# Optimization experiments

Hardware: AMD Instinct MI355X
Metric: run time of the kernel (lower is better)

## Reference

```python
import jax, jax.numpy as jnp
import numpy as np

B, D_IN, UNITS = 8192, 4096, 4096

def setup_inputs() -> dict:
    key = jax.random.key(0)
    k1, k2 = jax.random.split(key)
    x = jax.random.normal(k1, (B, D_IN), dtype=jnp.float32)
    w = jax.random.normal(k2, (D_IN, UNITS), dtype=jnp.float32)
    b = jnp.zeros((UNITS,), dtype=jnp.float32)
    return {"x": x, "w": w, "b": b}

def reference(x, w, b):
    # Bipolar dense: sign-binarize the weights, full-precision matmul, bias, relu.
    weights = jnp.sign(w)  # values in {-1, 0, +1}; matches tf.math.sign
    out = jnp.matmul(x, weights) + b  # [B, UNITS]
    return jax.nn.relu(out)
```

## Files before the change

kernel.cpp:

```cpp
#include <hip/hip_runtime.h>
#include <hip/hip_bf16.h>
#include <stdint.h>

#define M_DIM 8192
#define N_DIM 4096
#define K_DIM 4096

typedef __attribute__((ext_vector_type(4))) int   int4v;
typedef __attribute__((ext_vector_type(4))) float floatx4;

__global__ __launch_bounds__(256) void quant_x_kernel(const float* __restrict__ x,
                                                      signed char* __restrict__ xq,
                                                      float* __restrict__ xs) {
    const int row = blockIdx.x;
    const int tid = threadIdx.x;
    const int wave = tid >> 6, lane = tid & 63;
    const float4* xr = (const float4*)(x + (size_t)row * K_DIM);

    float4 v[4];
    float m = 0.f;
    #pragma unroll
    for (int j = 0; j < 4; ++j) {
        v[j] = xr[j * 256 + tid];
        m = fmaxf(m, fmaxf(fmaxf(fabsf(v[j].x), fabsf(v[j].y)),
                           fmaxf(fabsf(v[j].z), fabsf(v[j].w))));
    }
    #pragma unroll
    for (int off = 32; off >= 1; off >>= 1) m = fmaxf(m, __shfl_down(m, off));
    __shared__ float wm[4];
    if (lane == 0) wm[wave] = m;
    __syncthreads();
    const float M = fmaxf(fmaxf(wm[0], wm[1]), fmaxf(wm[2], wm[3]));
    const float inv = M > 0.f ? 127.f / M : 0.f;
    if (tid == 0) xs[row] = M > 0.f ? M / 127.f : 0.f;

    char4* xo = (char4*)(xq + (size_t)row * K_DIM);
    #pragma unroll
    for (int j = 0; j < 4; ++j) {
        char4 q;
        q.x = (signed char)__float2int_rn(v[j].x * inv);
        q.y = (signed char)__float2int_rn(v[j].y * inv);
        q.z = (signed char)__float2int_rn(v[j].z * inv);
        q.w = (signed char)__float2int_rn(v[j].w * inv);
        xo[j * 256 + tid] = q;
    }
}

__global__ __launch_bounds__(256) void cvt_w_kernel(const float* __restrict__ w,
                                                    signed char* __restrict__ wT) {
    __shared__ signed char tile[64][68];
    const int t  = threadIdx.x;
    const int k0 = blockIdx.y * 64;
    const int n0 = blockIdx.x * 64;
    #pragma unroll
    for (int p = 0; p < 4; ++p) {
        int kk = p * 16 + (t >> 4);
        int nn = (t & 15) * 4;
        float4 v = *reinterpret_cast<const float4*>(&w[(size_t)(k0 + kk) * N_DIM + n0 + nn]);
        tile[kk][nn + 0] = v.x > 0.f ? 1 : (v.x < 0.f ? -1 : 0);
        tile[kk][nn + 1] = v.y > 0.f ? 1 : (v.y < 0.f ? -1 : 0);
        tile[kk][nn + 2] = v.z > 0.f ? 1 : (v.z < 0.f ? -1 : 0);
        tile[kk][nn + 3] = v.w > 0.f ? 1 : (v.w < 0.f ? -1 : 0);
    }
    __syncthreads();
    const int r = t >> 2;
    const int c = (t & 3) * 16;
    int4v o;
    signed char* op = (signed char*)&o;
    #pragma unroll
    for (int j = 0; j < 16; ++j) op[j] = tile[c + j][r];
    *reinterpret_cast<int4v*>(&wT[(size_t)(n0 + r) * K_DIM + k0 + c]) = o;
}

#define BM 256
#define BN 256
#define BK 64
#define NT (K_DIM / BK)

#define GLD(gsrc, ldst) __builtin_amdgcn_global_load_lds( \
    (const __attribute__((address_space(1))) unsigned int*)(gsrc), \
    (__attribute__((address_space(3))) unsigned int*)(ldst), 16, 0, 0)

__global__ __launch_bounds__(512, 2) void gemm_i8_kernel(
    const signed char* __restrict__ A,
    const signed char* __restrict__ BT,
    const float* __restrict__ xsc,
    const float* __restrict__ bias,
    float* __restrict__ C)
{
    __shared__ signed char As[3][2][128 * 64];
    __shared__ signed char Bs[3][2][128 * 64];

    const int tid  = threadIdx.x;
    const int wave = tid >> 6;
    const int lane = tid & 63;
    const int wm   = wave >> 2;
    const int wn   = wave & 3;
    const int bh   = wn >> 1;
    const int brow0 = (wn & 1) * 64;

    const int bid  = blockIdx.x;
    const int sbid = (bid & 7) * 64 + (bid >> 3);
    const int tn   = sbid & 15;
    const int tm   = sbid >> 4;
    const int bm   = tm * BM;
    const int bn   = tn * BN;

    const int srow = tid >> 2;
    const int scol = ((tid & 3) ^ ((tid >> 3) & 3)) * 16;

    const int laneRow = (lane & 15) * 64;
    const int colX = ((lane >> 4) * 16) ^ (((lane >> 1) & 3) << 4);

    int4v acc[8][4] = {};

#define STAGE_HALF(G, R0, KOFS, LDST) do { \
    GLD((G) + (size_t)((R0) + srow) * K_DIM + (KOFS) + scol, (LDST) + wave * 1024); \
  } while (0)

    STAGE_HALF(A,  bm,        0, As[0][0]);
    STAGE_HALF(A,  bm + 128,  0, As[0][1]);
    STAGE_HALF(BT, bn,        0, Bs[0][0]);
    STAGE_HALF(BT, bn + 128,  0, Bs[0][1]);
    STAGE_HALF(A,  bm,       BK, As[1][0]);
    STAGE_HALF(A,  bm + 128, BK, As[1][1]);
    STAGE_HALF(BT, bn,       BK, Bs[1][0]);
    STAGE_HALF(BT, bn + 128, BK, Bs[1][1]);
    asm volatile("s_waitcnt vmcnt(4)" ::: "memory");
    __builtin_amdgcn_s_barrier();

    int4v a[4];
    int4v a2[4];
    int4v b[4];

    int rd = 0;
    int st = 2;

    for (int t = 0; t < NT; ++t) {
        const char* Ar = (const char*)As[rd][wm];
        const char* Br = (const char*)Bs[rd][bh];
        const int kS = (t + 2 < NT ? t + 2 : NT - 1) * BK;

        a[0]  = *(const int4v*)(Ar + (0*16)*64 + laneRow + colX);
        b[0]  = *(const int4v*)(Br + (brow0 +  0)*64 + laneRow + colX);
        b[1]  = *(const int4v*)(Br + (brow0 + 16)*64 + laneRow + colX);
        b[2]  = *(const int4v*)(Br + (brow0 + 32)*64 + laneRow + colX);
        b[3]  = *(const int4v*)(Br + (brow0 + 48)*64 + laneRow + colX);
        a[1]  = *(const int4v*)(Ar + (1*16)*64 + laneRow + colX);
        a[2]  = *(const int4v*)(Ar + (2*16)*64 + laneRow + colX);
        a[3]  = *(const int4v*)(Ar + (3*16)*64 + laneRow + colX);
        a2[0] = *(const int4v*)(Ar + ((64 + 0*16))*64 + laneRow + colX);
        a2[1] = *(const int4v*)(Ar + ((64 + 1*16))*64 + laneRow + colX);
        a2[2] = *(const int4v*)(Ar + ((64 + 2*16))*64 + laneRow + colX);
        a2[3] = *(const int4v*)(Ar + ((64 + 3*16))*64 + laneRow + colX);

        STAGE_HALF(A,  bm,       kS, As[st][0]);
        STAGE_HALF(A,  bm + 128, kS, As[st][1]);
        STAGE_HALF(BT, bn,       kS, Bs[st][0]);
        STAGE_HALF(BT, bn + 128, kS, Bs[st][1]);

        __builtin_amdgcn_s_setprio(1);
        #pragma unroll
        for (int mf = 0; mf < 4; ++mf)
            #pragma unroll
            for (int nf = 0; nf < 4; ++nf)
                acc[mf][nf] = __builtin_amdgcn_mfma_i32_16x16x64_i8(
                    a[mf], b[nf], acc[mf][nf], 0, 0, 0);
        #pragma unroll
        for (int mf = 0; mf < 4; ++mf)
            #pragma unroll
            for (int nf = 0; nf < 4; ++nf)
                acc[4 + mf][nf] = __builtin_amdgcn_mfma_i32_16x16x64_i8(
                    a2[mf], b[nf], acc[4 + mf][nf], 0, 0, 0);
        __builtin_amdgcn_s_setprio(0);

        asm volatile("s_waitcnt vmcnt(4)" ::: "memory");
        __builtin_amdgcn_s_barrier();

        rd = (rd == 2) ? 0 : rd + 1;
        st = (st == 2) ? 0 : st + 1;
    }

    float bv[4];
    #pragma unroll
    for (int nf = 0; nf < 4; ++nf)
        bv[nf] = bias[bn + wn * 64 + nf * 16 + (lane & 15)];
    #pragma unroll
    for (int mf = 0; mf < 8; ++mf) {
        const int row0 = bm + wm * 128 + mf * 16 + (lane >> 4) * 4;
        float sr[4];
        #pragma unroll
        for (int r = 0; r < 4; ++r) sr[r] = xsc[row0 + r];
        #pragma unroll
        for (int nf = 0; nf < 4; ++nf) {
            const int col = bn + wn * 64 + nf * 16 + (lane & 15);
            float* cp = C + (size_t)row0 * N_DIM + col;
            #pragma unroll
            for (int r = 0; r < 4; ++r) {
                float v = (float)acc[mf][nf][r] * sr[r] + bv[nf];
                cp[(size_t)r * N_DIM] = v > 0.f ? v : 0.f;
            }
        }
    }
}

__global__ void naive_kernel(const float* __restrict__ x, const float* __restrict__ w,
                             const float* __restrict__ b, float* __restrict__ out) {
    __shared__ float xs[16][16];
    __shared__ float ws[16][17];
    const int row = blockIdx.y * 16 + threadIdx.y;
    const int col = blockIdx.x * 16 + threadIdx.x;
    float acc = 0.f;
    for (int k0 = 0; k0 < K_DIM; k0 += 16) {
        xs[threadIdx.y][threadIdx.x] = x[(size_t)row * K_DIM + k0 + threadIdx.x];
        float wv = w[(size_t)(k0 + threadIdx.y) * N_DIM + col];
        ws[threadIdx.y][threadIdx.x] = wv > 0.f ? 1.f : (wv < 0.f ? -1.f : 0.f);
        __syncthreads();
        #pragma unroll
        for (int kk = 0; kk < 16; ++kk) acc += xs[threadIdx.y][kk] * ws[kk][threadIdx.x];
        __syncthreads();
    }
    float v = acc + b[col];
    out[(size_t)row * N_DIM + col] = v > 0.f ? v : 0.f;
}

extern "C" void kernel_launch(void* const* d_in, const int* in_sizes, int n_in,
                              void* d_out, int out_size, void* d_ws, size_t ws_size,
                              hipStream_t stream) {
    const float* x = (const float*)d_in[0];
    const float* w = (const float*)d_in[1];
    const float* b = (const float*)d_in[2];
    float* out = (float*)d_out;

    const size_t xq_bytes = (size_t)M_DIM * K_DIM;
    const size_t wT_bytes = (size_t)K_DIM * N_DIM;
    const size_t xs_bytes = (size_t)M_DIM * sizeof(float);

    if (ws_size >= xq_bytes + wT_bytes + xs_bytes) {
        signed char* xq = (signed char*)d_ws;
        signed char* wT = (signed char*)((char*)d_ws + xq_bytes);
        float*       xs = (float*)((char*)d_ws + xq_bytes + wT_bytes);
        quant_x_kernel<<<M_DIM, 256, 0, stream>>>(x, xq, xs);
        cvt_w_kernel<<<dim3(N_DIM / 64, K_DIM / 64), 256, 0, stream>>>(w, wT);
        gemm_i8_kernel<<<(M_DIM / BM) * (N_DIM / BN), 512, 0, stream>>>(xq, wT, xs, b, out);
    } else {
        naive_kernel<<<dim3(N_DIM / 16, M_DIM / 16), dim3(16, 16), 0, stream>>>(x, w, b, out);
    }
}
```

Before: 183.0 us.

## Process two K-tiles per barrier using four-stage LDS ring buffer

The int8 GEMM main loop now consumes two BK=64 tiles per iteration from a four-slot LDS ring, up from three slots. It issues the global-to-LDS prefetch for the next two tiles before computing the current pair. The aim is to halve the number of block-wide barriers and waitcnt points per K sweep. In exchange, LDS use rises to 128 KB per block. Each iteration now waits with vmcnt(0), so the loads just issued must fully land before the barrier, which may expose memory latency that the old rolling vmcnt(4) scheme hid.

Measured after the change: 184.7 us. Within noise of the previous version (+0.9%).

```diff
diff --git a/kernel.cpp b/kernel.cpp
--- a/kernel.cpp
+++ b/kernel.cpp
@@ -88,8 +88,8 @@
     const float* __restrict__ bias,
     float* __restrict__ C)
 {
-    __shared__ signed char As[3][2][128 * 64];
-    __shared__ signed char Bs[3][2][128 * 64];
+    __shared__ signed char As[4][2][128 * 64];
+    __shared__ signed char Bs[4][2][128 * 64];
 
     const int tid  = threadIdx.x;
     const int wave = tid >> 6;
@@ -126,38 +126,77 @@
     STAGE_HALF(A,  bm + 128, BK, As[1][1]);
     STAGE_HALF(BT, bn,       BK, Bs[1][0]);
     STAGE_HALF(BT, bn + 128, BK, Bs[1][1]);
-    asm volatile("s_waitcnt vmcnt(4)" ::: "memory");
+    asm volatile("s_waitcnt vmcnt(0)" ::: "memory");
     __builtin_amdgcn_s_barrier();
 
     int4v a[4];
     int4v a2[4];
     int4v b[4];
 
-    int rd = 0;
-    int st = 2;
-
-    for (int t = 0; t < NT; ++t) {
-        const char* Ar = (const char*)As[rd][wm];
-        const char* Br = (const char*)Bs[rd][bh];
-        const int kS = (t + 2 < NT ? t + 2 : NT - 1) * BK;
-
-        a[0]  = *(const int4v*)(Ar + (0*16)*64 + laneRow + colX);
-        b[0]  = *(const int4v*)(Br + (brow0 +  0)*64 + laneRow + colX);
-        b[1]  = *(const int4v*)(Br + (brow0 + 16)*64 + laneRow + colX);
-        b[2]  = *(const int4v*)(Br + (brow0 + 32)*64 + laneRow + colX);
-        b[3]  = *(const int4v*)(Br + (brow0 + 48)*64 + laneRow + colX);
-        a[1]  = *(const int4v*)(Ar + (1*16)*64 + laneRow + colX);
-        a[2]  = *(const int4v*)(Ar + (2*16)*64 + laneRow + colX);
-        a[3]  = *(const int4v*)(Ar + (3*16)*64 + laneRow + colX);
-        a2[0] = *(const int4v*)(Ar + ((64 + 0*16))*64 + laneRow + colX);
-        a2[1] = *(const int4v*)(Ar + ((64 + 1*16))*64 + laneRow + colX);
-        a2[2] = *(const int4v*)(Ar + ((64 + 2*16))*64 + laneRow + colX);
-        a2[3] = *(const int4v*)(Ar + ((64 + 3*16))*64 + laneRow + colX);
-
-        STAGE_HALF(A,  bm,       kS, As[st][0]);
-        STAGE_HALF(A,  bm + 128, kS, As[st][1]);
-        STAGE_HALF(BT, bn,       kS, Bs[st][0]);
-        STAGE_HALF(BT, bn + 128, kS, Bs[st][1]);
+#define SUBTILE(SLOT) do { \
+    const char* Ar = (const char*)As[SLOT][wm]; \
+    const char* Br = (const char*)Bs[SLOT][bh]; \
+    a[0]  = *(const int4v*)(Ar + (0*16)*64 + laneRow + colX); \
+    b[0]  = *(const int4v*)(Br + (brow0 +  0)*64 + laneRow + colX); \
+    b[1]  = *(const int4v*)(Br + (brow0 + 16)*64 + laneRow + colX); \
+    b[2]  = *(const int4v*)(Br + (brow0 + 32)*64 + laneRow + colX); \
+    b[3]  = *(const int4v*)(Br + (brow0 + 48)*64 + laneRow + colX); \
+    a[1]  = *(const int4v*)(Ar + (1*16)*64 + laneRow + colX); \
+    a[2]  = *(const int4v*)(Ar + (2*16)*64 + laneRow + colX); \
+    a[3]  = *(const int4v*)(Ar + (3*16)*64 + laneRow + colX); \
+    a2[0] = *(const int4v*)(Ar + ((64 + 0*16))*64 + laneRow + colX); \
+    a2[1] = *(const int4v*)(Ar + ((64 + 1*16))*64 + laneRow + colX); \
+    a2[2] = *(const int4v*)(Ar + ((64 + 2*16))*64 + laneRow + colX); \
+    a2[3] = *(const int4v*)(Ar + ((64 + 3*16))*64 + laneRow + colX); \
+    __builtin_amdgcn_s_setprio(1); \
+    _Pragma("unroll") \
+    for (int mf = 0; mf < 4; ++mf) \
+        _Pragma("unroll") \
+        for (int nf = 0; nf < 4; ++nf) \
+            acc[mf][nf] = __builtin_amdgcn_mfma_i32_16x16x64_i8( \
+                a[mf], b[nf], acc[mf][nf], 0, 0, 0); \
+    _Pragma("unroll") \
+    for (int mf = 0; mf < 4; ++mf) \
+        _Pragma("unroll") \
+        for (int nf = 0; nf < 4; ++nf) \
+            acc[4 + mf][nf] = __builtin_amdgcn_mfma_i32_16x16x64_i8( \
+                a2[mf], b[nf], acc[4 + mf][nf], 0, 0, 0); \
+    __builtin_amdgcn_s_setprio(0); \
+  } while (0)
+
+    for (int t = 0; t < NT; t += 2) {
+        const int s0 = t & 3;
+        const int s1 = (t + 1) & 3;
+        const int s2 = (t + 2) & 3;
+        const int s3 = (t + 3) & 3;
+        const int k2 = (t + 2 < NT ? t + 2 : NT - 1) * BK;
+        const int k3 = (t + 3 < NT ? t + 3 : NT - 1) * BK;
+
+        {
+            const char* Ar = (const char*)As[s0][wm];
+            const char* Br = (const char*)Bs[s0][bh];
+            a[0]  = *(const int4v*)(Ar + (0*16)*64 + laneRow + colX);
+            b[0]  = *(const int4v*)(Br + (brow0 +  0)*64 + laneRow + colX);
+            b[1]  = *(const int4v*)(Br + (brow0 + 16)*64 + laneRow + colX);
+            b[2]  = *(const int4v*)(Br + (brow0 + 32)*64 + laneRow + colX);
+            b[3]  = *(const int4v*)(Br + (brow0 + 48)*64 + laneRow + colX);
+            a[1]  = *(const int4v*)(Ar + (1*16)*64 + laneRow + colX);
+            a[2]  = *(const int4v*)(Ar + (2*16)*64 + laneRow + colX);
+            a[3]  = *(const int4v*)(Ar + (3*16)*64 + laneRow + colX);
+            a2[0] = *(const int4v*)(Ar + ((64 + 0*16))*64 + laneRow + colX);
+            a2[1] = *(const int4v*)(Ar + ((64 + 1*16))*64 + laneRow + colX);
+            a2[2] = *(const int4v*)(Ar + ((64 + 2*16))*64 + laneRow + colX);
+            a2[3] = *(const int4v*)(Ar + ((64 + 3*16))*64 + laneRow + colX);
+        }
+
+        STAGE_HALF(A,  bm,       k2, As[s2][0]);
+        STAGE_HALF(A,  bm + 128, k2, As[s2][1]);
+        STAGE_HALF(BT, bn,       k2, Bs[s2][0]);
+        STAGE_HALF(BT, bn + 128, k2, Bs[s2][1]);
+        STAGE_HALF(A,  bm,       k3, As[s3][0]);
+        STAGE_HALF(A,  bm + 128, k3, As[s3][1]);
+        STAGE_HALF(BT, bn,       k3, Bs[s3][0]);
+        STAGE_HALF(BT, bn + 128, k3, Bs[s3][1]);
 
         __builtin_amdgcn_s_setprio(1);
         #pragma unroll
@@ -174,11 +213,10 @@
                     a2[mf], b[nf], acc[4 + mf][nf], 0, 0, 0);
         __builtin_amdgcn_s_setprio(0);
 
-        asm volatile("s_waitcnt vmcnt(4)" ::: "memory");
+        SUBTILE(s1);
+
+        asm volatile("s_waitcnt vmcnt(0)" ::: "memory");
         __builtin_amdgcn_s_barrier();
-
-        rd = (rd == 2) ? 0 : rd + 1;
-        st = (st == 2) ? 0 : st + 1;
     }
 
     float bv[4];
```

## Double GEMM block to 1024 threads with 64x64 per-wave tiles

Applied to the files above, without the earlier changes.

The int8 GEMM kernel now runs 16 waves per 256x256 block instead of 8. Each wave computes a 64x64 sub-tile instead of 128x64, so accumulator registers are halved and each thread issues one global-to-LDS load per operand per stage. The aim is more resident waves to hide memory and LDS latency. In exchange, per-wave data reuse drops: more LDS reads per MFMA. The aggressive launch bound (1024, 4) may also push the compiler into tight register limits or spills.

Result: no change. 180.0 us (-1.6%).

```diff
diff --git a/kernel.cpp b/kernel.cpp
--- a/kernel.cpp
+++ b/kernel.cpp
@@ -27,10 +27,10 @@
     }
     #pragma unroll
     for (int off = 32; off >= 1; off >>= 1) m = fmaxf(m, __shfl_down(m, off));
-    __shared__ float wm[4];
-    if (lane == 0) wm[wave] = m;
+    __shared__ float wm_s[4];
+    if (lane == 0) wm_s[wave] = m;
     __syncthreads();
-    const float M = fmaxf(fmaxf(wm[0], wm[1]), fmaxf(wm[2], wm[3]));
+    const float M = fmaxf(fmaxf(wm_s[0], wm_s[1]), fmaxf(wm_s[2], wm_s[3]));
     const float inv = M > 0.f ? 127.f / M : 0.f;
     if (tid == 0) xs[row] = M > 0.f ? M / 127.f : 0.f;
 
@@ -81,23 +81,21 @@
     (const __attribute__((address_space(1))) unsigned int*)(gsrc), \
     (__attribute__((address_space(3))) unsigned int*)(ldst), 16, 0, 0)
 
-__global__ __launch_bounds__(512, 2) void gemm_i8_kernel(
+__global__ __launch_bounds__(1024, 4) void gemm_i8_kernel(
     const signed char* __restrict__ A,
     const signed char* __restrict__ BT,
     const float* __restrict__ xsc,
     const float* __restrict__ bias,
     float* __restrict__ C)
 {
-    __shared__ signed char As[3][2][128 * 64];
-    __shared__ signed char Bs[3][2][128 * 64];
+    __shared__ signed char As[3][256 * 64];
+    __shared__ signed char Bs[3][256 * 64];
 
     const int tid  = threadIdx.x;
     const int wave = tid >> 6;
     const int lane = tid & 63;
     const int wm   = wave >> 2;
     const int wn   = wave & 3;
-    const int bh   = wn >> 1;
-    const int brow0 = (wn & 1) * 64;
 
     const int bid  = blockIdx.x;
     const int sbid = (bid & 7) * 64 + (bid >> 3);
@@ -111,53 +109,44 @@
 
     const int laneRow = (lane & 15) * 64;
     const int colX = ((lane >> 4) * 16) ^ (((lane >> 1) & 3) << 4);
-
-    int4v acc[8][4] = {};
-
-#define STAGE_HALF(G, R0, KOFS, LDST) do { \
-    GLD((G) + (size_t)((R0) + srow) * K_DIM + (KOFS) + scol, (LDST) + wave * 1024); \
+    const int Abase = wm * 64 * 64;
+    const int Bbase = wn * 64 * 64;
+
+    int4v acc[4][4] = {};
+
+#define STAGE_T(G, R0, KOFS, LDSLOT) do { \
+    GLD((G) + (size_t)((R0) + srow) * K_DIM + (KOFS) + scol, (LDSLOT) + wave * 1024); \
   } while (0)
 
-    STAGE_HALF(A,  bm,        0, As[0][0]);
-    STAGE_HALF(A,  bm + 128,  0, As[0][1]);
-    STAGE_HALF(BT, bn,        0, Bs[0][0]);
-    STAGE_HALF(BT, bn + 128,  0, Bs[0][1]);
-    STAGE_HALF(A,  bm,       BK, As[1][0]);
-    STAGE_HALF(A,  bm + 128, BK, As[1][1]);
-    STAGE_HALF(BT, bn,       BK, Bs[1][0]);
-    STAGE_HALF(BT, bn + 128, BK, Bs[1][1]);
-    asm volatile("s_waitcnt vmcnt(4)" ::: "memory");
+    STAGE_T(A,  bm, 0,  As[0]);
+    STAGE_T(BT, bn, 0,  Bs[0]);
+    STAGE_T(A,  bm, BK, As[1]);
+    STAGE_T(BT, bn, BK, Bs[1]);
+    asm volatile("s_waitcnt vmcnt(2)" ::: "memory");
     __builtin_amdgcn_s_barrier();
 
     int4v a[4];
-    int4v a2[4];
     int4v b[4];
 
     int rd = 0;
     int st = 2;
 
     for (int t = 0; t < NT; ++t) {
-        const char* Ar = (const char*)As[rd][wm];
-        const char* Br = (const char*)Bs[rd][bh];
+        const char* Ar = (const char*)As[rd];
+        const char* Br = (const char*)Bs[rd];
         const int kS = (t + 2 < NT ? t + 2 : NT - 1) * BK;
 
-        a[0]  = *(const int4v*)(Ar + (0*16)*64 + laneRow + colX);
-        b[0]  = *(const int4v*)(Br + (brow0 +  0)*64 + laneRow + colX);
-        b[1]  = *(const int4v*)(Br + (brow0 + 16)*64 + laneRow + colX);
-        b[2]  = *(const int4v*)(Br + (brow0 + 32)*64 + laneRow + colX);
-        b[3]  = *(const int4v*)(Br + (brow0 + 48)*64 + laneRow + colX);
-        a[1]  = *(const int4v*)(Ar + (1*16)*64 + laneRow + colX);
-        a[2]  = *(const int4v*)(Ar + (2*16)*64 + laneRow + colX);
-        a[3]  = *(const int4v*)(Ar + (3*16)*64 + laneRow + colX);
-        a2[0] = *(const int4v*)(Ar + ((64 + 0*16))*64 + laneRow + colX);
-        a2[1] = *(const int4v*)(Ar + ((64 + 1*16))*64 + laneRow + colX);
-        a2[2] = *(const int4v*)(Ar + ((64 + 2*16))*64 + laneRow + colX);
-        a2[3] = *(const int4v*)(Ar + ((64 + 3*16))*64 + laneRow + colX);
-
-        STAGE_HALF(A,  bm,       kS, As[st][0]);
-        STAGE_HALF(A,  bm + 128, kS, As[st][1]);
-        STAGE_HALF(BT, bn,       kS, Bs[st][0]);
-        STAGE_HALF(BT, bn + 128, kS, Bs[st][1]);
+        a[0] = *(const int4v*)(Ar + Abase + (0*16)*64 + laneRow + colX);
+        b[0] = *(const int4v*)(Br + Bbase + (0*16)*64 + laneRow + colX);
+        b[1] = *(const int4v*)(Br + Bbase + (1*16)*64 + laneRow + colX);
+        b[2] = *(const int4v*)(Br + Bbase + (2*16)*64 + laneRow + colX);
+        b[3] = *(const int4v*)(Br + Bbase + (3*16)*64 + laneRow + colX);
+        a[1] = *(const int4v*)(Ar + Abase + (1*16)*64 + laneRow + colX);
+        a[2] = *(const int4v*)(Ar + Abase + (2*16)*64 + laneRow + colX);
+        a[3] = *(const int4v*)(Ar + Abase + (3*16)*64 + laneRow + colX);
+
+        STAGE_T(A,  bm, kS, As[st]);
+        STAGE_T(BT, bn, kS, Bs[st]);
 
         __builtin_amdgcn_s_setprio(1);
         #pragma unroll
@@ -166,15 +155,9 @@
             for (int nf = 0; nf < 4; ++nf)
                 acc[mf][nf] = __builtin_amdgcn_mfma_i32_16x16x64_i8(
                     a[mf], b[nf], acc[mf][nf], 0, 0, 0);
-        #pragma unroll
-        for (int mf = 0; mf < 4; ++mf)
-            #pragma unroll
-            for (int nf = 0; nf < 4; ++nf)
-                acc[4 + mf][nf] = __builtin_amdgcn_mfma_i32_16x16x64_i8(
-                    a2[mf], b[nf], acc[4 + mf][nf], 0, 0, 0);
         __builtin_amdgcn_s_setprio(0);
 
-        asm volatile("s_waitcnt vmcnt(4)" ::: "memory");
+        asm volatile("s_waitcnt vmcnt(2)" ::: "memory");
         __builtin_amdgcn_s_barrier();
 
         rd = (rd == 2) ? 0 : rd + 1;
@@ -186,8 +169,8 @@
     for (int nf = 0; nf < 4; ++nf)
         bv[nf] = bias[bn + wn * 64 + nf * 16 + (lane & 15)];
     #pragma unroll
-    for (int mf = 0; mf < 8; ++mf) {
-        const int row0 = bm + wm * 128 + mf * 16 + (lane >> 4) * 4;
+    for (int mf = 0; mf < 4; ++mf) {
+        const int row0 = bm + wm * 64 + mf * 16 + (lane >> 4) * 4;
         float sr[4];
         #pragma unroll
         for (int r = 0; r < 4; ++r) sr[r] = xsc[row0 + r];
@@ -242,7 +225,7 @@
         float*       xs = (float*)((char*)d_ws + xq_bytes + wT_bytes);
         quant_x_kernel<<<M_DIM, 256, 0, stream>>>(x, xq, xs);
         cvt_w_kernel<<<dim3(N_DIM / 64, K_DIM / 64), 256, 0, stream>>>(w, wT);
-        gemm_i8_kernel<<<(M_DIM / BM) * (N_DIM / BN), 512, 0, stream>>>(xq, wT, xs, b, out);
+        gemm_i8_kernel<<<(M_DIM / BM) * (N_DIM / BN), 1024, 0, stream>>>(xq, wT, xs, b, out);
     } else {
         naive_kernel<<<dim3(N_DIM / 16, M_DIM / 16), dim3(16, 16), 0, stream>>>(x, w, b, out);
     }
```
